# Performance work log

Hardware: AMD Instinct MI355X
Metric: run time of the kernel (lower is better)

## Reference

```python
import jax, jax.numpy as jnp
import numpy as np

MARGIN = 0.3
WARMUP_EPOCHS = 10
K = 5
ALPHA = 2.0
SAME_CAM_NEG_BOOST = 1.2
NEG_INF = jnp.float32(-jnp.inf)
POS_INF = jnp.float32(jnp.inf)


def setup_inputs() -> dict:
    key = jax.random.key(0)
    k1, k2, k3 = jax.random.split(key, 3)
    N, D = 8192, 2048
    feats = jax.random.normal(k1, (N, D), dtype=jnp.float32)
    labels = jax.random.randint(k2, (N,), 0, 256, dtype=jnp.int64)
    camids = jax.random.randint(k3, (N,), 0, 8, dtype=jnp.int64)
    return {"feats": feats, "labels": labels, "camids": camids, "epoch": 20}


def _topk_mean(dist_mat, mask, k, largest):
    # dist_mat [N,N], mask [N,N] bool. Per-row mean of k largest/smallest valid elems.
    if largest:
        work = jnp.where(mask, dist_mat, NEG_INF)
        vals, _ = jax.lax.top_k(work, k)            # [N,k] largest
        fallback = jnp.max(work, axis=1)
    else:
        work = jnp.where(mask, dist_mat, POS_INF)
        vals = -jax.lax.top_k(-work, k)[0]          # [N,k] smallest
        fallback = jnp.min(work, axis=1)
    is_valid = jnp.isfinite(vals)
    safe_sum = jnp.sum(jnp.where(is_valid, vals, 0.0), axis=1)
    counts = jnp.maximum(is_valid.sum(axis=1), 1)
    mean = safe_sum / counts
    return jnp.where(is_valid.any(axis=1), mean, fallback)


def _forward(feats, labels, camids, epoch):
    # (1) L2 normalize
    norm = jnp.linalg.norm(feats, axis=-1, keepdims=True)
    x = feats / jnp.maximum(norm, 1e-12)
    # Euclidean distance matrix [N,N]
    sq = jnp.sum(x * x, axis=1)
    dist2 = sq[:, None] + sq[None, :] - 2.0 * (x @ x.T)
    dist = jnp.sqrt(jnp.maximum(dist2, 1e-12))
    # masks (constants w.r.t. grad)
    N = feats.shape[0]
    eye = jnp.eye(N, dtype=bool)
    same_label = labels[:, None] == labels[None, :]
    same_cam = camids[:, None] == camids[None, :]
    is_pos = same_label & ~eye & ~same_cam   # cross_cam_pos=True
    is_neg = ~same_label & ~eye
    # boosted same-camera negatives
    neg_bias = jnp.where(is_neg & same_cam, SAME_CAM_NEG_BOOST, 1.0)
    dist_neg_sel = dist / jnp.maximum(neg_bias, 1e-6)
    # (2) top-k hard mining
    d_ap = _topk_mean(dist, is_pos, K, largest=True)
    d_an = _topk_mean(dist_neg_sel, is_neg, K, largest=False)
    # (5) hardness-aware weighting (no grad)
    w = jax.lax.stop_gradient(jax.nn.sigmoid(ALPHA * (d_ap - d_an)))
    w = w / jnp.maximum(w.mean(), 1e-12)
    # (3) margin schedule
    if epoch is not None and epoch < WARMUP_EPOCHS:
        per_sample = jax.nn.softplus(-(d_an - d_ap))
    else:
        per_sample = jax.nn.relu(d_ap - d_an + MARGIN)  # MarginRankingLoss, y=1
    loss = jnp.mean(w * per_sample)
    return loss, jax.lax.stop_gradient(d_ap), jax.lax.stop_gradient(d_an)


def reference(feats, labels, camids, epoch):
    return _forward(feats, labels, camids, epoch)
```

## Files before the change

### kernel.cpp

```cpp
#include <hip/hip_runtime.h>
#include <hip/hip_bf16.h>
#include <stdint.h>

typedef float   floatx4  __attribute__((ext_vector_type(4)));
typedef float   floatx16 __attribute__((ext_vector_type(16)));
typedef int     intx4    __attribute__((ext_vector_type(4)));
typedef int     intx8    __attribute__((ext_vector_type(8)));
typedef _Float16 halfx8  __attribute__((ext_vector_type(8)));
typedef _Float16 halfx4  __attribute__((ext_vector_type(4)));
typedef _Float16 half2v  __attribute__((ext_vector_type(2)));

#define NROW 8192
#define NDIM 2048
#define BM 128
#define SLICE 64
#define NSLICE 32
#define NSTRIP 64
#define NTILE (NSTRIP*(NSTRIP+1)/2)
#define NPOSB 256
#define DT_LD 136
#define KL_SYM 64
#define SLOT_P 8
#define MERGE_BLOCKS 256
#define BOOST_INV 0.6944444444f
#define XBT_STRIP 262144
#define XBT_SLICE 8192

__device__ __forceinline__ void ins_desc(float (&a)[5], float v) {
#pragma unroll
    for (int k = 0; k < 5; ++k) { float hi = fmaxf(a[k], v); float lo = fminf(a[k], v); a[k] = hi; v = lo; }
}
__device__ __forceinline__ void ins_asc(float (&a)[5], float v) {
#pragma unroll
    for (int k = 0; k < 5; ++k) { float lo = fminf(a[k], v); float hi = fmaxf(a[k], v); a[k] = lo; v = hi; }
}

__device__ __forceinline__ int   h2bits(half2v v) { return __builtin_bit_cast(int, v); }
__device__ __forceinline__ half2v bits2h(int v)   { return __builtin_bit_cast(half2v, v); }
__device__ __forceinline__ void ins_desc2(half2v (&a)[5], half2v v) {
#pragma unroll
    for (int k = 0; k < 5; ++k) {
        half2v hi = __builtin_elementwise_max(a[k], v);
        half2v lo = __builtin_elementwise_min(a[k], v);
        a[k] = hi; v = lo;
    }
}
__device__ __forceinline__ void ins_asc2(half2v (&a)[5], half2v v) {
#pragma unroll
    for (int k = 0; k < 5; ++k) {
        half2v lo = __builtin_elementwise_min(a[k], v);
        half2v hi = __builtin_elementwise_max(a[k], v);
        a[k] = lo; v = hi;
    }
}

__device__ __forceinline__ void load_lds16(const void* g, void* l) {
    __builtin_amdgcn_global_load_lds((__attribute__((address_space(1))) void*)(void*)g,
                                     (__attribute__((address_space(3))) void*)l,
                                     16, 0, 0);
}

__global__ __launch_bounds__(256) void k_normalize(const float* __restrict__ feats,
                                                   unsigned char* __restrict__ xb,
                                                   unsigned char* __restrict__ xbt,
                                                   float* __restrict__ sq) {
    const int lane = threadIdx.x & 63;
    const int row = (blockIdx.x << 2) + (threadIdx.x >> 6);
    const float* f = feats + (size_t)row * NDIM;
    float4 v[8];
    float ss = 0.f;
#pragma unroll
    for (int i = 0; i < 8; ++i) {
        v[i] = *(const float4*)(f + ((i << 6) + lane) * 4);
        ss += v[i].x * v[i].x + v[i].y * v[i].y + v[i].z * v[i].z + v[i].w * v[i].w;
    }
#pragma unroll
    for (int o = 32; o > 0; o >>= 1) ss += __shfl_xor(ss, o);
    float inv = 1.0f / fmaxf(sqrtf(ss), 1e-12f);
    if (lane == 0) sq[row] = ss * inv * inv;
    unsigned char* xo = xb + (size_t)row * NDIM;
    const int strip = row >> 7, rr = row & 127, g = rr >> 5, m32r = rr & 31;
    unsigned char* bt = xbt + (size_t)strip * XBT_STRIP + g * 2048 + m32r * 32
                      + ((lane >> 4) * XBT_SLICE) + (((lane >> 3) & 1) * 1024) + 4 * (lane & 7);
#pragma unroll
    for (int i = 0; i < 8; ++i) {
        int w0 = __builtin_amdgcn_cvt_pk_fp8_f32(v[i].x * inv, v[i].y * inv, 0, false);
        w0     = __builtin_amdgcn_cvt_pk_fp8_f32(v[i].z * inv, v[i].w * inv, w0, true);
        *(int*)(xo + ((i << 6) + lane) * 4) = w0;
        *(int*)(bt + (size_t)4 * i * XBT_SLICE) = w0;
    }
}

__device__ __forceinline__ void scan_half_row_neg(const _Float16* Dt_,
        int srow, int shalf, float (&neg5)[5]) {
    const int s2 = 2 * (srow & 7);
    const int PINF2 = 0x7C007C00;
    half2v n5[5];
#pragma unroll
    for (int k = 0; k < 5; ++k) n5[k] = bits2h(PINF2);
#pragma unroll
    for (int c8 = 0; c8 < 8; ++c8) {
        const int pc = ((shalf * 8 + c8) + s2) & 15;
        intx4 v = *(const intx4*)(Dt_ + srow * DT_LD + pc * 8);
#pragma unroll
        for (int e = 0; e < 4; ++e) ins_asc2(n5, bits2h(v[e]));
    }
    half2v tn[5];
#pragma unroll
    for (int k = 0; k < 5; ++k)
        tn[k] = bits2h((int)__builtin_amdgcn_alignbit((unsigned)h2bits(n5[k]), (unsigned)h2bits(n5[k]), 16));
#pragma unroll
    for (int k = 0; k < 5; ++k) ins_asc2(n5, tn[k]);
#pragma unroll
    for (int k = 0; k < 5; ++k) neg5[k] = (float)n5[k][0];
}

__device__ __forceinline__ void emit_neg(float (&neg5)[5], int shalf,
        _Float16* negp, int gi, int slot) {
    float tn[5];
#pragma unroll
    for (int k = 0; k < 5; ++k) tn[k] = __shfl_xor(neg5[k], 1);
#pragma unroll
    for (int k = 0; k < 5; ++k) { if (tn[k] < neg5[4]) ins_asc(neg5, tn[k]); }
    if (shalf == 0) {
        const float PINF = __builtin_inff();
        halfx8 hn;
#pragma unroll
        for (int k = 0; k < 5; ++k) hn[k] = (_Float16)neg5[k];
        hn[5] = hn[6] = hn[7] = (_Float16)PINF;
        *(halfx8*)(negp + ((size_t)slot * NROW + gi) * SLOT_P) = hn;
    }
}

__global__ __launch_bounds__(256, 3) void k_main(
        const unsigned char* __restrict__ xb, const unsigned char* __restrict__ xbt,
        const float* __restrict__ sq,
        const int* __restrict__ labels, const int* __restrict__ camids,
        _Float16* __restrict__ negp, _Float16* __restrict__ posf) {
    __shared__ __align__(16) char smem[36864];

    const int tid = threadIdx.x;
    const int w = tid >> 6, lane = tid & 63;
    const int m32 = lane & 31;
    const int hi = lane >> 5;
    const float FINF = __builtin_inff();
    const float NINF = -FINF;

    if (blockIdx.x < NPOSB) {
        char* stg0 = smem;
        _Float16* D2 = (_Float16*)(smem + 12288);
        int* mem = (int*)(smem + 21504);
        unsigned short* mlc = (unsigned short*)(smem + 21760);
        float* msq = (float*)(smem + 21888);
        int* cntp = (int*)(smem + 22144);

        const int key = (lane >> 1) & 3;
        const int p0 = ((2 * hi + key) & 3) * 16;
        const int p1 = ((2 * hi + 1 + key) & 3) * 16;

        const int L = blockIdx.x;
        if (tid == 0) *cntp = 0;
        __syncthreads();
        for (int i = tid; i < NROW; i += 256) {
            if (labels[i] == L) {
                int slot = atomicAdd(cntp, 1);
                if (slot < 64) mem[slot] = i;
            }
        }
        __syncthreads();
        const int cnt = min(*cntp, 64);
        if (tid < 64) {
            if (tid < cnt) {
                int gi = mem[tid];
                mlc[tid] = (unsigned short)((labels[gi] << 4) | camids[gi]);
                msq[tid] = sq[gi];
            } else {
                mem[tid] = 0; mlc[tid] = 0xFFFF; msq[tid] = 0.f;
            }
        }
        __syncthreads();

        const int wm = w >> 1, wn = w & 1;
        const int lr = lane >> 2;
        const int lcb = (((lane & 3) - ((lane >> 3) & 3)) & 3) * 16;
        const int myrow = mem[w * 16 + lr];

        auto pstage = [&](int buf, int koff) {
            load_lds16(xb + (size_t)myrow * NDIM + koff + lcb,
                       stg0 + (buf << 12) + w * 1024);
        };

        floatx16 acc;
#pragma unroll
        for (int r = 0; r < 16; ++r) acc[r] = 0.f;

        pstage(0, 0);
        pstage(1, SLICE);
        for (int s = 0; s < NSLICE; ++s) {
            if (s + 2 < NSLICE) pstage((s + 2) % 3, (s + 2) * SLICE);
            if (s < NSLICE - 2)       asm volatile("s_waitcnt vmcnt(2)" ::: "memory");
            else if (s == NSLICE - 2) asm volatile("s_waitcnt vmcnt(1)" ::: "memory");
            else                      asm volatile("s_waitcnt vmcnt(0)" ::: "memory");
            __builtin_amdgcn_s_barrier();
            asm volatile("" ::: "memory");
            const char* Ab = stg0 + ((s % 3) << 12);
            const char* ap = Ab + (wm * 32 + m32) * SLICE;
            intx4 alo = *(const intx4*)(ap + p0);
            intx4 ahi = *(const intx4*)(ap + p1);
            intx8 af = __builtin_shufflevector(alo, ahi, 0, 1, 2, 3, 4, 5, 6, 7);
            const char* bp = Ab + (wn * 32 + m32) * SLICE;
            intx4 blo = *(const intx4*)(bp + p0);
            intx4 bhi = *(const intx4*)(bp + p1);
            intx8 bf = __builtin_shufflevector(blo, bhi, 0, 1, 2, 3, 4, 5, 6, 7);
            acc = __builtin_amdgcn_mfma_scale_f32_32x32x64_f8f6f4(af, bf, acc, 0, 0, 0, 127, 0, 127);
            asm volatile("" ::: "memory");
            __builtin_amdgcn_s_barrier();
            asm volatile("" ::: "memory");
        }

        {
            const int jl = (w & 1) * 32 + m32;
            const int lcj = (int)mlc[jl];
            const float sj = msq[jl];
            const int wm2 = w >> 1;
#pragma unroll
            for (int r = 0; r < 16; ++r) {
                const int il = wm2 * 32 + (r & 3) + 8 * (r >> 2) + 4 * hi;
                float d2 = fmaxf(msq[il] + sj - 2.0f * acc[r], 1e-12f);
                const int x = (int)mlc[il] ^ lcj;
                bool posv = ((x & 0xFFF0) == 0) & ((x & 15) != 0);
                D2[il * 72 + jl] = posv ? (_Float16)d2 : (_Float16)NINF;
            }
        }
        __syncthreads();

        {
            const int prow = tid >> 2, q = tid & 3;
            const int NINF2 = 0xFC00FC00;
            half2v p5h[5];
#pragma unroll
            for (int k = 0; k < 5; ++k) p5h[k] = bits2h(NINF2);
            const _Float16* dp = D2 + prow * 72 + q * 16;
            intx4 v0 = *(const intx4*)dp;
            intx4 v1 = *(const intx4*)(dp + 8);
#pragma unroll
            for (int e = 0; e < 4; ++e) ins_desc2(p5h, bits2h(v0[e]));
#pragma unroll
            for (int e = 0; e < 4; ++e) ins_desc2(p5h, bits2h(v1[e]));
            half2v tp[5];
#pragma unroll
            for (int k = 0; k < 5; ++k)
                tp[k] = bits2h((int)__builtin_amdgcn_alignbit((unsigned)h2bits(p5h[k]), (unsigned)h2bits(p5h[k]), 16));
#pragma unroll
            for (int k = 0; k < 5; ++k) ins_desc2(p5h, tp[k]);
            float p5[5];
#pragma unroll
            for (int k = 0; k < 5; ++k) p5[k] = (float)p5h[k][0];
#pragma unroll
            for (int o = 1; o <= 2; o <<= 1) {
                float tq[5];
#pragma unroll
                for (int k = 0; k < 5; ++k) tq[k] = __shfl_xor(p5[k], o);
#pragma unroll
                for (int k = 0; k < 5; ++k) { if (tq[k] > p5[4]) ins_desc(p5, tq[k]); }
            }
            if (q == 0 && prow < cnt) {
                halfx8 hp;
#pragma unroll
                for (int k = 0; k < 5; ++k) hp[k] = (_Float16)p5[k];
                hp[5] = hp[6] = hp[7] = (_Float16)NINF;
                *(halfx8*)(posf + (size_t)mem[prow] * SLOT_P) = hp;
            }
        }
        return;
    }

    _Float16* Dt = (_Float16*)smem;
    float* sqr_s = (float*)(smem + 34816);
    float* sqc_s = sqr_s + BM;
    unsigned short* labcam_a = (unsigned short*)(sqc_s + BM);
    unsigned short* labcam_b = labcam_a + BM;

    const int wm = w >> 1, wn = w & 1;

    int a, b;
    {
        int bx = blockIdx.x - NPOSB;
        int o = (bx & 7) * (NTILE / 8) + (bx >> 3);
        if (o < 1792) {
            int st = o >> 6;
            int SA = (int)((1.0f + sqrtf(8.0f * (float)st + 1.0f)) * 0.5f);
            while (SA * (SA - 1) / 2 > st) --SA;
            while (SA * (SA + 1) / 2 <= st) ++SA;
            int SB = st - SA * (SA - 1) / 2;
            int inner = o & 63;
            a = SA * 8 + (inner >> 3);
            b = SB * 8 + (inner & 7);
        } else {
            int idx = o - 1792;
            int st = idx / 36;
            int inner = idx - st * 36;
            int ia = (int)((sqrtf(8.0f * (float)inner + 1.0f) - 1.0f) * 0.5f);
            while (ia * (ia + 1) / 2 > inner) --ia;
            while ((ia + 1) * (ia + 2) / 2 <= inner) ++ia;
            int ib = inner - ia * (ia + 1) / 2;
            a = st * 8 + ia;
            b = st * 8 + ib;
        }
    }
    const int r0 = a * BM, c0 = b * BM;

    if (tid < BM) {
        int gi = r0 + tid;
        sqr_s[tid] = sq[gi];
        labcam_a[tid] = (unsigned short)((labels[gi] << 4) | camids[gi]);
    } else {
        int t2 = tid - BM;
        int gj = c0 + t2;
        sqc_s[t2] = sq[gj];
        labcam_b[t2] = (unsigned short)((labels[gj] << 4) | camids[gj]);
    }
    __syncthreads();

    const unsigned char* aptr0 = xbt + (size_t)a * XBT_STRIP + (2 * wm) * 2048 + lane * 32;
    const unsigned char* aptr1 = aptr0 + 2048;
    const unsigned char* bptr0 = xbt + (size_t)b * XBT_STRIP + (2 * wn) * 2048 + lane * 32;
    const unsigned char* bptr1 = bptr0 + 2048;

    intx4 xa0, xa1, xa2, xa3, xq0, xq1, xq2, xq3;
    intx4 ya0, ya1, ya2, ya3, yq0, yq1, yq2, yq3;

    xa0 = *(const intx4*)(aptr0);       xa1 = *(const intx4*)(aptr0 + 16);
    xa2 = *(const intx4*)(aptr1);       xa3 = *(const intx4*)(aptr1 + 16);
    xq0 = *(const intx4*)(bptr0);       xq1 = *(const intx4*)(bptr0 + 16);
    xq2 = *(const intx4*)(bptr1);       xq3 = *(const intx4*)(bptr1 + 16);
    ya0 = *(const intx4*)(aptr0 + XBT_SLICE); ya1 = *(const intx4*)(aptr0 + XBT_SLICE + 16);
    ya2 = *(const intx4*)(aptr1 + XBT_SLICE); ya3 = *(const intx4*)(aptr1 + XBT_SLICE + 16);
    yq0 = *(const intx4*)(bptr0 + XBT_SLICE); yq1 = *(const intx4*)(bptr0 + XBT_SLICE + 16);
    yq2 = *(const intx4*)(bptr1 + XBT_SLICE); yq3 = *(const intx4*)(bptr1 + XBT_SLICE + 16);

    const int srow = tid >> 1;
    const int shalf = tid & 1;

    floatx16 acc[2][2];
#pragma unroll
    for (int ti = 0; ti < 2; ++ti)
#pragma unroll
        for (int tj = 0; tj < 2; ++tj)
#pragma unroll
            for (int r = 0; r < 16; ++r) acc[ti][tj][r] = 0.f;

    for (int s = 0; s < NSLICE; s += 2) {
        {
            intx8 af0 = __builtin_shufflevector(xa0, xa1, 0, 1, 2, 3, 4, 5, 6, 7);
            intx8 af1 = __builtin_shufflevector(xa2, xa3, 0, 1, 2, 3, 4, 5, 6, 7);
            intx8 bf0 = __builtin_shufflevector(xq0, xq1, 0, 1, 2, 3, 4, 5, 6, 7);
            intx8 bf1 = __builtin_shufflevector(xq2, xq3, 0, 1, 2, 3, 4, 5, 6, 7);
            __builtin_amdgcn_s_setprio(1);
            acc[0][0] = __builtin_amdgcn_mfma_scale_f32_32x32x64_f8f6f4(af0, bf0, acc[0][0], 0, 0, 0, 127, 0, 127);
            acc[0][1] = __builtin_amdgcn_mfma_scale_f32_32x32x64_f8f6f4(af0, bf1, acc[0][1], 0, 0, 0, 127, 0, 127);
            acc[1][0] = __builtin_amdgcn_mfma_scale_f32_32x32x64_f8f6f4(af1, bf0, acc[1][0], 0, 0, 0, 127, 0, 127);
            acc[1][1] = __builtin_amdgcn_mfma_scale_f32_32x32x64_f8f6f4(af1, bf1, acc[1][1], 0, 0, 0, 127, 0, 127);
            __builtin_amdgcn_s_setprio(0);
        }
        if (s + 2 < NSLICE) {
            const size_t ko = (size_t)(s + 2) * XBT_SLICE;
            xa0 = *(const intx4*)(aptr0 + ko); xa1 = *(const intx4*)(aptr0 + ko + 16);
            xa2 = *(const intx4*)(aptr1 + ko); xa3 = *(const intx4*)(aptr1 + ko + 16);
            xq0 = *(const intx4*)(bptr0 + ko); xq1 = *(const intx4*)(bptr0 + ko + 16);
            xq2 = *(const intx4*)(bptr1 + ko); xq3 = *(const intx4*)(bptr1 + ko + 16);
        }
        {
            intx8 af0 = __builtin_shufflevector(ya0, ya1, 0, 1, 2, 3, 4, 5, 6, 7);
            intx8 af1 = __builtin_shufflevector(ya2, ya3, 0, 1, 2, 3, 4, 5, 6, 7);
            intx8 bf0 = __builtin_shufflevector(yq0, yq1, 0, 1, 2, 3, 4, 5, 6, 7);
            intx8 bf1 = __builtin_shufflevector(yq2, yq3, 0, 1, 2, 3, 4, 5, 6, 7);
            __builtin_amdgcn_s_setprio(1);
            acc[0][0] = __builtin_amdgcn_mfma_scale_f32_32x32x64_f8f6f4(af0, bf0, acc[0][0], 0, 0, 0, 127, 0, 127);
            acc[0][1] = __builtin_amdgcn_mfma_scale_f32_32x32x64_f8f6f4(af0, bf1, acc[0][1], 0, 0, 0, 127, 0, 127);
            acc[1][0] = __builtin_amdgcn_mfma_scale_f32_32x32x64_f8f6f4(af1, bf0, acc[1][0], 0, 0, 0, 127, 0, 127);
            acc[1][1] = __builtin_amdgcn_mfma_scale_f32_32x32x64_f8f6f4(af1, bf1, acc[1][1], 0, 0, 0, 127, 0, 127);
            __builtin_amdgcn_s_setprio(0);
        }
        if (s + 3 < NSLICE) {
            const size_t ko = (size_t)(s + 3) * XBT_SLICE;
            ya0 = *(const intx4*)(aptr0 + ko); ya1 = *(const intx4*)(aptr0 + ko + 16);
            ya2 = *(const intx4*)(aptr1 + ko); ya3 = *(const intx4*)(aptr1 + ko + 16);
            yq0 = *(const intx4*)(bptr0 + ko); yq1 = *(const intx4*)(bptr0 + ko + 16);
            yq2 = *(const intx4*)(bptr1 + ko); yq3 = *(const intx4*)(bptr1 + ko + 16);
        }
    }

    {
        const int jl0 = wn * 64 + m32, jl1 = jl0 + 32;
        const float sj0 = sqc_s[jl0], sj1 = sqc_s[jl1];
        const int lb0 = (int)labcam_b[jl0], lb1 = (int)labcam_b[jl1];
        const int jc0 = jl0 >> 3, j7_0 = jl0 & 7;
        const int jc1 = jl1 >> 3, j7_1 = jl1 & 7;
#pragma unroll
        for (int ti = 0; ti < 2; ++ti) {
#pragma unroll
            for (int r = 0; r < 16; ++r) {
                const int il = wm * 64 + ti * 32 + (r & 3) + 8 * (r >> 2) + 4 * hi;
                const float si = sqr_s[il];
                const int la = (int)labcam_a[il];
                const int rot = 2 * (il & 7);
                _Float16* drow = Dt + il * DT_LD;

                float d2 = fmaxf(si + sj0 - 2.0f * acc[ti][0][r], 1e-12f);
                int x = la ^ lb0;
                float nv = (x & 15) ? d2 : d2 * BOOST_INV;
                nv = (x & 0xFFF0) ? nv : FINF;
                acc[ti][0][r] = nv;
                drow[(((jc0 + rot) & 15) << 3) + j7_0] = (_Float16)nv;

                d2 = fmaxf(si + sj1 - 2.0f * acc[ti][1][r], 1e-12f);
                x = la ^ lb1;
                nv = (x & 15) ? d2 : d2 * BOOST_INV;
                nv = (x & 0xFFF0) ? nv : FINF;
                acc[ti][1][r] = nv;
                drow[(((jc1 + rot) & 15) << 3) + j7_1] = (_Float16)nv;
            }
        }
    }
    __syncthreads();

    float neg5[5];
    scan_half_row_neg(Dt, srow, shalf, neg5);
    emit_neg(neg5, shalf, negp, r0 + srow, b);

    if (a != b) {
        __syncthreads();
#pragma unroll
        for (int tj = 0; tj < 2; ++tj) {
#pragma unroll
            for (int ti = 0; ti < 2; ++ti) {
                const int jl = wn * 64 + tj * 32 + m32;
                const int cw2 = 2 * (jl & 7);
#pragma unroll
                for (int rq = 0; rq < 4; ++rq) {
                    const int base_row = wm * 64 + ti * 32 + 8 * rq + 4 * hi;
                    halfx4 h;
#pragma unroll
                    for (int e = 0; e < 4; ++e) h[e] = (_Float16)acc[ti][tj][rq * 4 + e];
                    const int pch = (((base_row >> 3) + cw2) & 15);
                    *(halfx4*)(Dt + jl * DT_LD + (pch << 3) + 4 * hi) = h;
                }
            }
        }
        __syncthreads();
        scan_half_row_neg(Dt, srow, shalf, neg5);
        emit_neg(neg5, shalf, negp, c0 + srow, a);
    }
}

__global__ __launch_bounds__(256) void k_merge_sym(const _Float16* __restrict__ negp,
        const _Float16* __restrict__ posf, const int* __restrict__ epoch_p,
        float* __restrict__ out, float* __restrict__ wsum_p, float* __restrict__ wpsum_p) {
    const int t = threadIdx.x;
    const int rl = t & 31;
    const int sg = t >> 5;
    const int row = blockIdx.x * 32 + rl;
    const float NINF = -__builtin_inff(), PINF = __builtin_inff();
    float n5[5] = {PINF, PINF, PINF, PINF, PINF};
    const size_t rbase = (size_t)row * SLOT_P;
#pragma unroll
    for (int s = 0; s < 8; ++s) {
        const size_t off = (size_t)(sg * 8 + s) * ((size_t)NROW * SLOT_P) + rbase;
        halfx8 nv = *(const halfx8*)(negp + off);
#pragma unroll
        for (int e = 0; e < 8; ++e) { float f = (float)nv[e]; if (f < n5[4]) ins_asc(n5, f); }
    }
    __shared__ __align__(16) _Float16 ln[32][8][8];
    const int sw = (sg + rl) & 7;
    {
        halfx8 hn;
#pragma unroll
        for (int k = 0; k < 5; ++k) hn[k] = (_Float16)n5[k];
        hn[5] = hn[6] = hn[7] = (_Float16)PINF;
        *(halfx8*)&ln[rl][sw][0] = hn;
    }
    __syncthreads();
    if (t < 32) {
        float N5[5] = {PINF, PINF, PINF, PINF, PINF};
#pragma unroll
        for (int g = 0; g < 8; ++g) {
            halfx8 nv = *(const halfx8*)&ln[t][g][0];
#pragma unroll
            for (int e = 0; e < 8; ++e) { float f = (float)nv[e]; if (f < N5[4]) ins_asc(N5, f); }
        }
        const int orow = blockIdx.x * 32 + t;
        halfx8 pv = *(const halfx8*)(posf + (size_t)orow * SLOT_P);
        float s = 0.f; int c = 0;
#pragma unroll
        for (int k = 0; k < 5; ++k) { float f = (float)pv[k]; bool fin = (f > NINF); s += fin ? sqrtf(f) : 0.f; c += fin ? 1 : 0; }
        float d_ap = (c > 0) ? s / (float)c : NINF;
        s = 0.f; c = 0;
#pragma unroll
        for (int k = 0; k < 5; ++k) { bool fin = (N5[k] < PINF); s += fin ? sqrtf(N5[k]) : 0.f; c += fin ? 1 : 0; }
        float d_an = (c > 0) ? s / (float)c : PINF;

        out[1 + orow] = d_ap;
        out[1 + NROW + orow] = d_an;
        float diff = d_ap - d_an;
        float w0 = 1.0f / (1.0f + expf(-2.0f * diff));
        float p;
        if (*epoch_p < 10) {
            p = fmaxf(diff, 0.0f) + log1pf(expf(-fabsf(diff)));
        } else {
            p = fmaxf(diff + 0.3f, 0.0f);
        }
        float wp = w0 * p;
#pragma unroll
        for (int o = 16; o > 0; o >>= 1) { w0 += __shfl_down(w0, o, 32); wp += __shfl_down(wp, o, 32); }
        if (t == 0) { wsum_p[blockIdx.x] = w0; wpsum_p[blockIdx.x] = wp; }
    }
}

__global__ void k_finalize(const float* __restrict__ wsum_p, const float* __restrict__ wpsum_p,
                           float* __restrict__ out) {
    const int t = threadIdx.x;
    float sw  = wsum_p[t] + wsum_p[t + 64] + wsum_p[t + 128] + wsum_p[t + 192];
    float swp = wpsum_p[t] + wpsum_p[t + 64] + wpsum_p[t + 128] + wpsum_p[t + 192];
#pragma unroll
    for (int o = 32; o > 0; o >>= 1) { sw += __shfl_down(sw, o); swp += __shfl_down(swp, o); }
    if (t == 0) {
        float M = fmaxf(sw / (float)NROW, 1e-12f);
        out[0] = swp / ((float)NROW * M);
    }
}

extern "C" void kernel_launch(void* const* d_in, const int* in_sizes, int n_in,
                              void* d_out, int out_size, void* d_ws, size_t ws_size,
                              hipStream_t stream) {
    const float* feats  = (const float*)d_in[0];
    const int*   labels = (const int*)d_in[1];
    const int*   camids = (const int*)d_in[2];
    const int*   epoch  = (const int*)d_in[3];
    float* out = (float*)d_out;
    char* ws = (char*)d_ws;

    unsigned char* xb  = (unsigned char*)ws;
    unsigned char* xbt = (unsigned char*)(ws + 16777216);
    float* sq = (float*)(ws + 33554432);
    const size_t NEG_HALVES = (size_t)KL_SYM * NROW * SLOT_P;
    _Float16* negp = (_Float16*)(ws + 33554432 + 32768);
    _Float16* posf = negp + NEG_HALVES;
    float* wsum_p  = (float*)((char*)(posf + (size_t)NROW * SLOT_P));
    float* wpsum_p = wsum_p + MERGE_BLOCKS;

    k_normalize<<<NROW / 4, 256, 0, stream>>>(feats, xb, xbt, sq);
    k_main<<<NPOSB + NTILE, 256, 0, stream>>>(xb, xbt, sq, labels, camids, negp, posf);
    k_merge_sym<<<MERGE_BLOCKS, 256, 0, stream>>>(negp, posf, epoch, out, wsum_p, wpsum_p);
    k_finalize<<<1, 64, 0, stream>>>(wsum_p, wpsum_p, out);
}
```

Measured before the change: 205.4 us.

## Drop row-major fp8 copy, read positive-pair operands from tiled layout, fuse finalize

The normalize kernel no longer writes the row-major fp8 copy of the features. The positive-pair blocks now load MFMA operands straight from the tiled xbt layout into registers with a two-slice software prefetch, replacing the LDS-staged triple-buffered pipeline and its barriers. The separate finalize kernel is folded into the merge kernel through atomic accumulation and a last-block ticket, which also removes one launch. This saves 16 MB of writes and a kernel launch, but positive blocks now issue scattered direct global loads without LDS reuse, and the float atomics make the sum order nondeterministic.

New measurement: 211.2 us. 1.03x slower.

```diff
diff --git a/kernel.cpp b/kernel.cpp
--- a/kernel.cpp
+++ b/kernel.cpp
@@ -54,16 +54,11 @@
     }
 }
 
-__device__ __forceinline__ void load_lds16(const void* g, void* l) {
-    __builtin_amdgcn_global_load_lds((__attribute__((address_space(1))) void*)(void*)g,
-                                     (__attribute__((address_space(3))) void*)l,
-                                     16, 0, 0);
-}
-
 __global__ __launch_bounds__(256) void k_normalize(const float* __restrict__ feats,
-                                                   unsigned char* __restrict__ xb,
                                                    unsigned char* __restrict__ xbt,
-                                                   float* __restrict__ sq) {
+                                                   float* __restrict__ sq,
+                                                   float* __restrict__ fz) {
+    if (blockIdx.x == 0 && threadIdx.x < 4) fz[threadIdx.x] = 0.f;
     const int lane = threadIdx.x & 63;
     const int row = (blockIdx.x << 2) + (threadIdx.x >> 6);
     const float* f = feats + (size_t)row * NDIM;
@@ -78,7 +73,6 @@
     for (int o = 32; o > 0; o >>= 1) ss += __shfl_xor(ss, o);
     float inv = 1.0f / fmaxf(sqrtf(ss), 1e-12f);
     if (lane == 0) sq[row] = ss * inv * inv;
-    unsigned char* xo = xb + (size_t)row * NDIM;
     const int strip = row >> 7, rr = row & 127, g = rr >> 5, m32r = rr & 31;
     unsigned char* bt = xbt + (size_t)strip * XBT_STRIP + g * 2048 + m32r * 32
                       + ((lane >> 4) * XBT_SLICE) + (((lane >> 3) & 1) * 1024) + 4 * (lane & 7);
@@ -86,7 +80,6 @@
     for (int i = 0; i < 8; ++i) {
         int w0 = __builtin_amdgcn_cvt_pk_fp8_f32(v[i].x * inv, v[i].y * inv, 0, false);
         w0     = __builtin_amdgcn_cvt_pk_fp8_f32(v[i].z * inv, v[i].w * inv, w0, true);
-        *(int*)(xo + ((i << 6) + lane) * 4) = w0;
         *(int*)(bt + (size_t)4 * i * XBT_SLICE) = w0;
     }
 }
@@ -133,7 +126,7 @@
 }
 
 __global__ __launch_bounds__(256, 3) void k_main(
-        const unsigned char* __restrict__ xb, const unsigned char* __restrict__ xbt,
+        const unsigned char* __restrict__ xbt,
         const float* __restrict__ sq,
         const int* __restrict__ labels, const int* __restrict__ camids,
         _Float16* __restrict__ negp, _Float16* __restrict__ posf) {
@@ -145,18 +138,14 @@
     const int hi = lane >> 5;
     const float FINF = __builtin_inff();
     const float NINF = -FINF;
+    const int wm = w >> 1, wn = w & 1;
 
     if (blockIdx.x < NPOSB) {
-        char* stg0 = smem;
-        _Float16* D2 = (_Float16*)(smem + 12288);
-        int* mem = (int*)(smem + 21504);
-        unsigned short* mlc = (unsigned short*)(smem + 21760);
-        float* msq = (float*)(smem + 21888);
-        int* cntp = (int*)(smem + 22144);
-
-        const int key = (lane >> 1) & 3;
-        const int p0 = ((2 * hi + key) & 3) * 16;
-        const int p1 = ((2 * hi + 1 + key) & 3) * 16;
+        _Float16* D2 = (_Float16*)smem;
+        int* mem = (int*)(smem + 9216);
+        unsigned short* mlc = (unsigned short*)(smem + 9472);
+        float* msq = (float*)(smem + 9600);
+        int* cntp = (int*)(smem + 9856);
 
         const int L = blockIdx.x;
         if (tid == 0) *cntp = 0;
@@ -180,52 +169,52 @@
         }
         __syncthreads();
 
-        const int wm = w >> 1, wn = w & 1;
-        const int lr = lane >> 2;
-        const int lcb = (((lane & 3) - ((lane >> 3) & 3)) & 3) * 16;
-        const int myrow = mem[w * 16 + lr];
-
-        auto pstage = [&](int buf, int koff) {
-            load_lds16(xb + (size_t)myrow * NDIM + koff + lcb,
-                       stg0 + (buf << 12) + w * 1024);
-        };
+        const int arow = mem[wm * 32 + m32];
+        const int brow = mem[wn * 32 + m32];
+        const unsigned char* ap = xbt + (size_t)(arow >> 7) * XBT_STRIP
+                                + ((arow >> 5) & 3) * 2048 + hi * 1024 + (arow & 31) * 32;
+        const unsigned char* bp = xbt + (size_t)(brow >> 7) * XBT_STRIP
+                                + ((brow >> 5) & 3) * 2048 + hi * 1024 + (brow & 31) * 32;
 
         floatx16 acc;
 #pragma unroll
         for (int r = 0; r < 16; ++r) acc[r] = 0.f;
 
-        pstage(0, 0);
-        pstage(1, SLICE);
-        for (int s = 0; s < NSLICE; ++s) {
-            if (s + 2 < NSLICE) pstage((s + 2) % 3, (s + 2) * SLICE);
-            if (s < NSLICE - 2)       asm volatile("s_waitcnt vmcnt(2)" ::: "memory");
-            else if (s == NSLICE - 2) asm volatile("s_waitcnt vmcnt(1)" ::: "memory");
-            else                      asm volatile("s_waitcnt vmcnt(0)" ::: "memory");
-            __builtin_amdgcn_s_barrier();
-            asm volatile("" ::: "memory");
-            const char* Ab = stg0 + ((s % 3) << 12);
-            const char* ap = Ab + (wm * 32 + m32) * SLICE;
-            intx4 alo = *(const intx4*)(ap + p0);
-            intx4 ahi = *(const intx4*)(ap + p1);
-            intx8 af = __builtin_shufflevector(alo, ahi, 0, 1, 2, 3, 4, 5, 6, 7);
-            const char* bp = Ab + (wn * 32 + m32) * SLICE;
-            intx4 blo = *(const intx4*)(bp + p0);
-            intx4 bhi = *(const intx4*)(bp + p1);
-            intx8 bf = __builtin_shufflevector(blo, bhi, 0, 1, 2, 3, 4, 5, 6, 7);
-            acc = __builtin_amdgcn_mfma_scale_f32_32x32x64_f8f6f4(af, bf, acc, 0, 0, 0, 127, 0, 127);
-            asm volatile("" ::: "memory");
-            __builtin_amdgcn_s_barrier();
-            asm volatile("" ::: "memory");
+        intx4 xa0, xa1, xb0, xb1, ya0, ya1, yb0, yb1;
+        xa0 = *(const intx4*)(ap);              xa1 = *(const intx4*)(ap + 16);
+        xb0 = *(const intx4*)(bp);              xb1 = *(const intx4*)(bp + 16);
+        ya0 = *(const intx4*)(ap + XBT_SLICE);  ya1 = *(const intx4*)(ap + XBT_SLICE + 16);
+        yb0 = *(const intx4*)(bp + XBT_SLICE);  yb1 = *(const intx4*)(bp + XBT_SLICE + 16);
+        for (int s = 0; s < NSLICE; s += 2) {
+            {
+                intx8 af = __builtin_shufflevector(xa0, xa1, 0, 1, 2, 3, 4, 5, 6, 7);
+                intx8 bf = __builtin_shufflevector(xb0, xb1, 0, 1, 2, 3, 4, 5, 6, 7);
+                acc = __builtin_amdgcn_mfma_scale_f32_32x32x64_f8f6f4(af, bf, acc, 0, 0, 0, 127, 0, 127);
+            }
+            if (s + 2 < NSLICE) {
+                const size_t ko = (size_t)(s + 2) * XBT_SLICE;
+                xa0 = *(const intx4*)(ap + ko); xa1 = *(const intx4*)(ap + ko + 16);
+                xb0 = *(const intx4*)(bp + ko); xb1 = *(const intx4*)(bp + ko + 16);
+            }
+            {
+                intx8 af = __builtin_shufflevector(ya0, ya1, 0, 1, 2, 3, 4, 5, 6, 7);
+                intx8 bf = __builtin_shufflevector(yb0, yb1, 0, 1, 2, 3, 4, 5, 6, 7);
+                acc = __builtin_amdgcn_mfma_scale_f32_32x32x64_f8f6f4(af, bf, acc, 0, 0, 0, 127, 0, 127);
+            }
+            if (s + 3 < NSLICE) {
+                const size_t ko = (size_t)(s + 3) * XBT_SLICE;
+                ya0 = *(const intx4*)(ap + ko); ya1 = *(const intx4*)(ap + ko + 16);
+                yb0 = *(const intx4*)(bp + ko); yb1 = *(const intx4*)(bp + ko + 16);
+            }
         }
 
         {
-            const int jl = (w & 1) * 32 + m32;
+            const int jl = wn * 32 + m32;
             const int lcj = (int)mlc[jl];
             const float sj = msq[jl];
-            const int wm2 = w >> 1;
 #pragma unroll
             for (int r = 0; r < 16; ++r) {
-                const int il = wm2 * 32 + (r & 3) + 8 * (r >> 2) + 4 * hi;
+                const int il = wm * 32 + (r & 3) + 8 * (r >> 2) + 4 * hi;
                 float d2 = fmaxf(msq[il] + sj - 2.0f * acc[r], 1e-12f);
                 const int x = (int)mlc[il] ^ lcj;
                 bool posv = ((x & 0xFFF0) == 0) & ((x & 15) != 0);
@@ -280,8 +269,6 @@
     float* sqc_s = sqr_s + BM;
     unsigned short* labcam_a = (unsigned short*)(sqc_s + BM);
     unsigned short* labcam_b = labcam_a + BM;
-
-    const int wm = w >> 1, wn = w & 1;
 
     int a, b;
     {
@@ -456,7 +443,7 @@
 
 __global__ __launch_bounds__(256) void k_merge_sym(const _Float16* __restrict__ negp,
         const _Float16* __restrict__ posf, const int* __restrict__ epoch_p,
-        float* __restrict__ out, float* __restrict__ wsum_p, float* __restrict__ wpsum_p) {
+        float* __restrict__ out, float* __restrict__ fz) {
     const int t = threadIdx.x;
     const int rl = t & 31;
     const int sg = t >> 5;
@@ -513,20 +500,18 @@
         float wp = w0 * p;
 #pragma unroll
         for (int o = 16; o > 0; o >>= 1) { w0 += __shfl_down(w0, o, 32); wp += __shfl_down(wp, o, 32); }
-        if (t == 0) { wsum_p[blockIdx.x] = w0; wpsum_p[blockIdx.x] = wp; }
-    }
-}
-
-__global__ void k_finalize(const float* __restrict__ wsum_p, const float* __restrict__ wpsum_p,
-                           float* __restrict__ out) {
-    const int t = threadIdx.x;
-    float sw  = wsum_p[t] + wsum_p[t + 64] + wsum_p[t + 128] + wsum_p[t + 192];
-    float swp = wpsum_p[t] + wpsum_p[t + 64] + wpsum_p[t + 128] + wpsum_p[t + 192];
-#pragma unroll
-    for (int o = 32; o > 0; o >>= 1) { sw += __shfl_down(sw, o); swp += __shfl_down(swp, o); }
-    if (t == 0) {
-        float M = fmaxf(sw / (float)NROW, 1e-12f);
-        out[0] = swp / ((float)NROW * M);
+        if (t == 0) {
+            atomicAdd(&fz[0], w0);
+            atomicAdd(&fz[1], wp);
+            __threadfence();
+            int tk = atomicAdd((int*)&fz[2], 1);
+            if (tk == MERGE_BLOCKS - 1) {
+                float sw2  = atomicAdd(&fz[0], 0.f);
+                float swp2 = atomicAdd(&fz[1], 0.f);
+                float M = fmaxf(sw2 / (float)NROW, 1e-12f);
+                out[0] = swp2 / ((float)NROW * M);
+            }
+        }
     }
 }
 
@@ -540,17 +525,14 @@
     float* out = (float*)d_out;
     char* ws = (char*)d_ws;
 
-    unsigned char* xb  = (unsigned char*)ws;
-    unsigned char* xbt = (unsigned char*)(ws + 16777216);
-    float* sq = (float*)(ws + 33554432);
+    unsigned char* xbt = (unsigned char*)ws;
+    float* sq = (float*)(ws + 16777216);
     const size_t NEG_HALVES = (size_t)KL_SYM * NROW * SLOT_P;
-    _Float16* negp = (_Float16*)(ws + 33554432 + 32768);
+    _Float16* negp = (_Float16*)(ws + 16777216 + 32768);
     _Float16* posf = negp + NEG_HALVES;
-    float* wsum_p  = (float*)((char*)(posf + (size_t)NROW * SLOT_P));
-    float* wpsum_p = wsum_p + MERGE_BLOCKS;
-
-    k_normalize<<<NROW / 4, 256, 0, stream>>>(feats, xb, xbt, sq);
-    k_main<<<NPOSB + NTILE, 256, 0, stream>>>(xb, xbt, sq, labels, camids, negp, posf);
-    k_merge_sym<<<MERGE_BLOCKS, 256, 0, stream>>>(negp, posf, epoch, out, wsum_p, wpsum_p);
-    k_finalize<<<1, 64, 0, stream>>>(wsum_p, wpsum_p, out);
-}
+    float* fz = (float*)((char*)(posf + (size_t)NROW * SLOT_P));
+
+    k_normalize<<<NROW / 4, 256, 0, stream>>>(feats, xbt, sq, fz);
+    k_main<<<NPOSB + NTILE, 256, 0, stream>>>(xbt, sq, labels, camids, negp, posf);
+    k_merge_sym<<<MERGE_BLOCKS, 256, 0, stream>>>(negp, posf, epoch, out, fz);
+}
```
